# Kernel tuning notes

Hardware: AMD Instinct MI355X
Metric: run time of the kernel (lower is better)

The kernel has to match this reference:

```python
import jax, jax.numpy as jnp
import numpy as np

N = 100000   # nodes
E = 3200000  # edges (avg degree 32)
F = 128      # node_features
H = 128      # GCN hidden
A = 1024     # num_actions
B = 256      # graphs in batch


def setup_inputs() -> dict:
    key = jax.random.key(0)
    ks = jax.random.split(key, 11)
    glorot = lambda k, shp: (jax.random.normal(k, shp, jnp.float32)
                             / np.sqrt(float(shp[0])))
    return {
        "x": jax.random.normal(ks[0], (N, F), jnp.float32),
        "edge_index": jax.random.randint(ks[1], (2, E), 0, N, dtype=jnp.int64),
        "batch": jnp.sort(jax.random.randint(ks[2], (N,), 0, B, dtype=jnp.int64)),
        "W1": glorot(ks[3], (F, H)), "b1": jnp.zeros((H,), jnp.float32),
        "W2": glorot(ks[4], (H, H)), "b2": jnp.zeros((H,), jnp.float32),
        "Wv": glorot(ks[5], (H, 1)), "bv": jnp.zeros((1,), jnp.float32),
        "Wp": glorot(ks[6], (H, A)), "bp": jnp.zeros((A,), jnp.float32),
    }


def reference(x, edge_index, batch, W1, b1, W2, b2, Wv, bv, Wp, bp):
    # --- GCN normalization (PyG gcn_norm with self-loops) ---
    loops = jnp.arange(N, dtype=edge_index.dtype)
    src = jnp.concatenate([edge_index[0], loops])  # [E+N] message sources
    dst = jnp.concatenate([edge_index[1], loops])  # [E+N] aggregation targets
    deg = jax.ops.segment_sum(jnp.ones(src.shape, jnp.float32), dst,
                              num_segments=N)       # in-degree incl. self-loop
    dinv = jax.lax.rsqrt(deg)                       # deg >= 1 due to self-loops
    norm = (dinv[src] * dinv[dst])[:, None]         # [E+N, 1]

    def gcn_conv(h, W, b):
        h = h @ W                                   # transform first (small GEMM)
        agg = jax.ops.segment_sum(h[src] * norm, dst, num_segments=N)
        return agg + b

    h = jax.nn.relu(gcn_conv(x, W1, b1))
    h = jax.nn.relu(gcn_conv(h, W2, b2))

    # --- global_mean_pool over graph ids ---
    counts = jax.ops.segment_sum(jnp.ones((N,), jnp.float32), batch,
                                 num_segments=B)
    pooled = jax.ops.segment_sum(h, batch, num_segments=B) \
             / jnp.maximum(counts, 1.0)[:, None]    # [B, H]

    v = jnp.tanh(pooled @ Wv + bv)                  # [B, 1]
    p = jax.nn.softmax(pooled @ Wp + bp, axis=-1)   # [B, A]
    return (v, p)
```

## Files before the change

### kernel.cpp

```cpp
#include <hip/hip_runtime.h>
#include <hip/hip_bf16.h>

#define GN 100000
#define GE 3200000
#define GH 128
#define GA 1024
#define GB 256

#define NBUK 391
#define BCAP 12288
#define B1BLK 5120
#define NBIN1 625

typedef __attribute__((ext_vector_type(8))) short short8v;
typedef __attribute__((ext_vector_type(4))) float f32x4v;

__device__ __forceinline__ unsigned int f2bf(float f) {
    unsigned int u = __float_as_uint(f);
    return (u + 0x7fffu + ((u >> 16) & 1u)) >> 16;
}
__device__ __forceinline__ float bflo(unsigned int u) { return __uint_as_float(u << 16); }
__device__ __forceinline__ float bfhi(unsigned int u) { return __uint_as_float(u & 0xffff0000u); }

__device__ __forceinline__ int wswz(int k, int n) {
    return (((k >> 5) * 8 + (n >> 4)) * 64 + ((k >> 3) & 3) * 16 + (n & 15)) * 8 + (k & 7);
}

__global__ __launch_bounds__(256) void k_prep(const float* __restrict__ W1,
                                              const float* __restrict__ W2,
                                              unsigned short* __restrict__ Wsw1,
                                              unsigned short* __restrict__ Wsw2,
                                              int* __restrict__ gcur) {
    int b = blockIdx.x, t = threadIdx.x;
    if (b < 64) {
        int idx = b * 256 + t;
        int k = idx >> 7, n = idx & 127;
        Wsw1[wswz(k, n)] = (unsigned short)f2bf(W1[idx]);
    } else if (b < 128) {
        int idx = (b - 64) * 256 + t;
        int k = idx >> 7, n = idx & 127;
        Wsw2[wswz(k, n)] = (unsigned short)f2bf(W2[idx]);
    } else {
        for (int i = t; i < NBUK; i += 256) gcur[i] = i * BCAP;
    }
}

__global__ __launch_bounds__(256) void k_bin1(const int* __restrict__ src,
                                              const int* __restrict__ dst,
                                              int* __restrict__ gcur,
                                              unsigned int* __restrict__ binned) {
    __shared__ int hist[512], lstart[512];
    __shared__ int curl[NBUK], gbase[NBUK];
    __shared__ unsigned int srec[B1BLK];
    __shared__ unsigned short sbuk[B1BLK];
    __shared__ int wsc[4];
    int t = threadIdx.x;
    hist[t] = 0; hist[t + 256] = 0;
    __syncthreads();
    int beg = blockIdx.x * B1BLK;
    unsigned int rec[20]; int bukv[20];
#pragma unroll
    for (int k = 0; k < 20; k++) {
        int e = beg + t + k * 256;
        int d = dst[e];
        rec[k] = (unsigned int)src[e] | ((unsigned int)(d & 255) << 17);
        bukv[k] = d >> 8;
        atomicAdd(&hist[bukv[k]], 1);
    }
    __syncthreads();
    int v0 = hist[2 * t], v1 = hist[2 * t + 1];
    int s = v0 + v1;
    int lane = t & 63, w = t >> 6;
    int x = s;
#pragma unroll
    for (int off = 1; off < 64; off <<= 1) {
        int y = __shfl_up(x, off);
        if (lane >= off) x += y;
    }
    if (lane == 63) wsc[w] = x;
    __syncthreads();
    int wo = 0;
#pragma unroll
    for (int i = 0; i < 4; i++)
        if (i < w) wo += wsc[i];
    int excl = wo + x - s;
    lstart[2 * t] = excl;
    lstart[2 * t + 1] = excl + v0;
    __syncthreads();
    for (int i = t; i < NBUK; i += 256) {
        curl[i] = lstart[i];
        int c = hist[i];
        gbase[i] = c ? atomicAdd(&gcur[i], c) : 0;
    }
    __syncthreads();
#pragma unroll
    for (int k = 0; k < 20; k++) {
        int p = atomicAdd(&curl[bukv[k]], 1);
        srec[p] = rec[k];
        sbuk[p] = (unsigned short)bukv[k];
    }
    __syncthreads();
    for (int i = t; i < B1BLK; i += 256) {
        int b = sbuk[i];
        binned[gbase[b] + (i - lstart[b])] = srec[i];
    }
}

__global__ __launch_bounds__(256) void k_sort2(const unsigned int* __restrict__ binned,
                                               const int* __restrict__ gcur,
                                               int* __restrict__ csr_src,
                                               int* __restrict__ nbeg,
                                               int* __restrict__ nend,
                                               float* __restrict__ dinv) {
    int b = blockIdx.x, t = threadIdx.x;
    __shared__ int hist[256], cur[256], wsum[4];
    hist[t] = 0;
    __syncthreads();
    int rbase = b * BCAP;
    int rend = gcur[b];
    for (int e = rbase + t; e < rend; e += 256)
        atomicAdd(&hist[(binned[e] >> 17) & 255], 1);
    __syncthreads();
    int h = hist[t];
    int lane = t & 63, w = t >> 6;
    int x = h;
#pragma unroll
    for (int off = 1; off < 64; off <<= 1) {
        int y = __shfl_up(x, off);
        if (lane >= off) x += y;
    }
    if (lane == 63) wsum[w] = x;
    __syncthreads();
    int wo = 0;
#pragma unroll
    for (int i = 0; i < 4; i++)
        if (i < w) wo += wsum[i];
    int excl = wo + x - h;
    int node = (b << 8) + t;
    if (node < GN) {
        nbeg[node] = rbase + excl;
        nend[node] = rbase + excl + h;
        dinv[node] = rsqrtf((float)(h + 1));
    }
    cur[t] = excl;
    __syncthreads();
    for (int e = rbase + t; e < rend; e += 256) {
        unsigned int v = binned[e];
        int dl = (v >> 17) & 255;
        int p = atomicAdd(&cur[dl], 1);
        csr_src[rbase + p] = (int)(v & 0x1FFFF);
    }
}

__global__ __launch_bounds__(256) void k_gemm1(const float* __restrict__ A,
                                               const unsigned short* __restrict__ Wsw,
                                               const float* __restrict__ dinv,
                                               unsigned int* __restrict__ C) {
    __shared__ float Ct[64][128];
    int t = threadIdx.x;
    int row0 = blockIdx.x * 64;
    int wv = t >> 6, lane = t & 63;
    int m16 = lane & 15, g = lane >> 4;
    f32x4v acc[8];
#pragma unroll
    for (int nb = 0; nb < 8; nb++) acc[nb] = (f32x4v){0.f, 0.f, 0.f, 0.f};
    int arow = row0 + wv * 16 + m16; if (arow >= GN) arow = GN - 1;
#pragma unroll
    for (int kb = 0; kb < 4; kb++) {
        const float* ap = &A[(size_t)arow * 128 + kb * 32 + g * 8];
        float4 a0 = *(const float4*)ap;
        float4 a1 = *(const float4*)(ap + 4);
        uint4 up;
        up.x = f2bf(a0.x) | (f2bf(a0.y) << 16);
        up.y = f2bf(a0.z) | (f2bf(a0.w) << 16);
        up.z = f2bf(a1.x) | (f2bf(a1.y) << 16);
        up.w = f2bf(a1.z) | (f2bf(a1.w) << 16);
        short8v af = *(short8v*)&up;
#pragma unroll
        for (int nb = 0; nb < 8; nb++) {
            short8v bf = *(const short8v*)&Wsw[((kb * 8 + nb) * 64 + lane) * 8];
            acc[nb] = __builtin_amdgcn_mfma_f32_16x16x32_bf16(af, bf, acc[nb], 0, 0, 0);
        }
    }
#pragma unroll
    for (int nb = 0; nb < 8; nb++)
#pragma unroll
        for (int r = 0; r < 4; r++)
            Ct[wv * 16 + g * 4 + r][nb * 16 + m16] = acc[nb][r];
    __syncthreads();
    int lr = t >> 2, ch = t & 3;
    int grow = row0 + lr;
    if (grow < GN) {
        float dv = dinv[grow];
#pragma unroll
        for (int q = 0; q < 4; q++) {
            int c0 = ch * 32 + q * 8;
            uint4 po;
            po.x = f2bf(Ct[lr][c0 + 0] * dv) | (f2bf(Ct[lr][c0 + 1] * dv) << 16);
            po.y = f2bf(Ct[lr][c0 + 2] * dv) | (f2bf(Ct[lr][c0 + 3] * dv) << 16);
            po.z = f2bf(Ct[lr][c0 + 4] * dv) | (f2bf(Ct[lr][c0 + 5] * dv) << 16);
            po.w = f2bf(Ct[lr][c0 + 6] * dv) | (f2bf(Ct[lr][c0 + 7] * dv) << 16);
            *(uint4*)&C[(size_t)grow * 64 + ch * 16 + q * 4] = po;
        }
    }
}

__global__ __launch_bounds__(256) void k_gemm2(const unsigned int* __restrict__ A,
                                               const unsigned short* __restrict__ Wsw,
                                               const float* __restrict__ dinv,
                                               unsigned int* __restrict__ C) {
    __shared__ float Ct[64][128];
    int t = threadIdx.x;
    int row0 = blockIdx.x * 64;
    int wv = t >> 6, lane = t & 63;
    int m16 = lane & 15, g = lane >> 4;
    f32x4v acc[8];
#pragma unroll
    for (int nb = 0; nb < 8; nb++) acc[nb] = (f32x4v){0.f, 0.f, 0.f, 0.f};
    int arow = row0 + wv * 16 + m16; if (arow >= GN) arow = GN - 1;
#pragma unroll
    for (int kb = 0; kb < 4; kb++) {
        uint4 av = *(const uint4*)&A[(size_t)arow * 64 + kb * 16 + g * 4];
        short8v af = *(short8v*)&av;
#pragma unroll
        for (int nb = 0; nb < 8; nb++) {
            short8v bf = *(const short8v*)&Wsw[((kb * 8 + nb) * 64 + lane) * 8];
            acc[nb] = __builtin_amdgcn_mfma_f32_16x16x32_bf16(af, bf, acc[nb], 0, 0, 0);
        }
    }
#pragma unroll
    for (int nb = 0; nb < 8; nb++)
#pragma unroll
        for (int r = 0; r < 4; r++)
            Ct[wv * 16 + g * 4 + r][nb * 16 + m16] = acc[nb][r];
    __syncthreads();
    int lr = t >> 2, ch = t & 3;
    int grow = row0 + lr;
    if (grow < GN) {
        float dv = dinv[grow];
#pragma unroll
        for (int q = 0; q < 4; q++) {
            int c0 = ch * 32 + q * 8;
            uint4 po;
            po.x = f2bf(Ct[lr][c0 + 0] * dv) | (f2bf(Ct[lr][c0 + 1] * dv) << 16);
            po.y = f2bf(Ct[lr][c0 + 2] * dv) | (f2bf(Ct[lr][c0 + 3] * dv) << 16);
            po.z = f2bf(Ct[lr][c0 + 4] * dv) | (f2bf(Ct[lr][c0 + 5] * dv) << 16);
            po.w = f2bf(Ct[lr][c0 + 6] * dv) | (f2bf(Ct[lr][c0 + 7] * dv) << 16);
            *(uint4*)&C[(size_t)grow * 64 + ch * 16 + q * 4] = po;
        }
    }
}

__global__ __launch_bounds__(256) void k_aggregate(const unsigned int* __restrict__ ts,
                                                   const int* __restrict__ nbeg,
                                                   const int* __restrict__ nend,
                                                   const int* __restrict__ csr_src,
                                                   const float* __restrict__ dinv,
                                                   const float* __restrict__ bias,
                                                   unsigned int* __restrict__ out) {
    int node = blockIdx.x * 4 + (threadIdx.x >> 6);
    if (node >= GN) return;
    int lane = threadIdx.x & 63;
    int beg = nbeg[node];
    int end = nend[node];
    float di = dinv[node];
    float ax = 0.f, ay = 0.f;
    for (int base = beg; base < end; base += 64) {
        int n = end - base; if (n > 64) n = 64;
        int myidx = (lane < n) ? csr_src[base + lane] : 0;
        int k = 0;
        for (; k + 16 <= n; k += 16) {
            unsigned int u[16];
#pragma unroll
            for (int q = 0; q < 16; q++) {
                int s = __shfl(myidx, k + q);
                u[q] = ts[s * 64 + lane];
            }
#pragma unroll
            for (int q = 0; q < 16; q++) { ax += bflo(u[q]); ay += bfhi(u[q]); }
        }
        for (; k + 4 <= n; k += 4) {
            unsigned int u[4];
#pragma unroll
            for (int q = 0; q < 4; q++) {
                int s = __shfl(myidx, k + q);
                u[q] = ts[s * 64 + lane];
            }
#pragma unroll
            for (int q = 0; q < 4; q++) { ax += bflo(u[q]); ay += bfhi(u[q]); }
        }
        for (; k < n; k++) {
            int s = __shfl(myidx, k);
            unsigned int u = ts[s * 64 + lane];
            ax += bflo(u); ay += bfhi(u);
        }
    }
    unsigned int su = ts[(size_t)node * 64 + lane];
    float bx = bias[lane * 2 + 0], by = bias[lane * 2 + 1];
    float ox = fmaxf(fmaf(di, ax + bflo(su), bx), 0.f);
    float oy = fmaxf(fmaf(di, ay + bfhi(su), by), 0.f);
    out[(size_t)node * 64 + lane] = f2bf(ox) | (f2bf(oy) << 16);
}

__global__ __launch_bounds__(256) void k_pool(const unsigned int* __restrict__ h,
                                              const int* __restrict__ batch,
                                              float* __restrict__ pooled) {
    int g = blockIdx.x;
    int t = threadIdx.x;
    int f = t & 63, part = t >> 6;
    int lo = 0, hi = GN;
    while (lo < hi) { int m = (lo + hi) >> 1; if (batch[m] < g) lo = m + 1; else hi = m; }
    int start = lo;
    hi = GN;
    while (lo < hi) { int m = (lo + hi) >> 1; if (batch[m] <= g) lo = m + 1; else hi = m; }
    int end = lo;
    float ax = 0.f, ay = 0.f;
    for (int i = start + part; i < end; i += 4) {
        unsigned int u = h[(size_t)i * 64 + f];
        ax += bflo(u); ay += bfhi(u);
    }
    __shared__ float redx[256], redy[256];
    redx[t] = ax; redy[t] = ay;
    __syncthreads();
    if (part == 0) {
        float sx = redx[f] + redx[f + 64] + redx[f + 128] + redx[f + 192];
        float sy = redy[f] + redy[f + 64] + redy[f + 128] + redy[f + 192];
        float inv = 1.0f / fmaxf((float)(end - start), 1.0f);
        pooled[g * 128 + 2 * f + 0] = sx * inv;
        pooled[g * 128 + 2 * f + 1] = sy * inv;
    }
}

__global__ void k_value(const float* __restrict__ pooled, const float* __restrict__ Wv,
                        const float* __restrict__ bv, float* __restrict__ out) {
    int g = threadIdx.x;
    const float4* p4 = (const float4*)(pooled + g * 128);
    const float4* w4 = (const float4*)Wv;
    float s = 0.f;
#pragma unroll 8
    for (int i = 0; i < 32; i++) {
        float4 a = p4[i], b = w4[i];
        s += a.x * b.x + a.y * b.y + a.z * b.z + a.w * b.w;
    }
    out[g] = tanhf(s + bv[0]);
}

__global__ __launch_bounds__(256) void k_policy(const float* __restrict__ pooled,
                                                const float* __restrict__ Wp,
                                                const float* __restrict__ bp,
                                                float* __restrict__ out) {
    int g0 = blockIdx.x * 4;
    int t = threadIdx.x;
    __shared__ float pr[4][128];
    __shared__ float red[256];
    if (t < 128) {
#pragma unroll
        for (int gg = 0; gg < 4; gg++)
            pr[gg][t] = pooled[(size_t)(g0 + gg) * 128 + t];
    }
    __syncthreads();
    float bb0 = bp[t], bb1 = bp[t + 256], bb2 = bp[t + 512], bb3 = bp[t + 768];
    float acc[4][4];
#pragma unroll
    for (int gg = 0; gg < 4; gg++) {
        acc[gg][0] = bb0; acc[gg][1] = bb1; acc[gg][2] = bb2; acc[gg][3] = bb3;
    }
    for (int k = 0; k < 128; k++) {
        const float* wr = Wp + (size_t)k * 1024;
        float w0 = wr[t], w1 = wr[t + 256], w2 = wr[t + 512], w3 = wr[t + 768];
#pragma unroll
        for (int gg = 0; gg < 4; gg++) {
            float pv = pr[gg][k];
            acc[gg][0] = fmaf(pv, w0, acc[gg][0]);
            acc[gg][1] = fmaf(pv, w1, acc[gg][1]);
            acc[gg][2] = fmaf(pv, w2, acc[gg][2]);
            acc[gg][3] = fmaf(pv, w3, acc[gg][3]);
        }
    }
#pragma unroll
    for (int gg = 0; gg < 4; gg++) {
        float m = fmaxf(fmaxf(acc[gg][0], acc[gg][1]), fmaxf(acc[gg][2], acc[gg][3]));
        red[t] = m;
        __syncthreads();
        for (int off = 128; off > 0; off >>= 1) {
            if (t < off) red[t] = fmaxf(red[t], red[t + off]);
            __syncthreads();
        }
        float mx = red[0];
        __syncthreads();
        float e0 = __expf(acc[gg][0] - mx), e1 = __expf(acc[gg][1] - mx);
        float e2 = __expf(acc[gg][2] - mx), e3 = __expf(acc[gg][3] - mx);
        red[t] = (e0 + e1) + (e2 + e3);
        __syncthreads();
        for (int off = 128; off > 0; off >>= 1) {
            if (t < off) red[t] += red[t + off];
            __syncthreads();
        }
        float inv = 1.0f / red[0];
        __syncthreads();
        size_t ob = (size_t)(g0 + gg) * 1024;
        out[ob + t + 0]   = e0 * inv;
        out[ob + t + 256] = e1 * inv;
        out[ob + t + 512] = e2 * inv;
        out[ob + t + 768] = e3 * inv;
    }
}

extern "C" void kernel_launch(void* const* d_in, const int* in_sizes, int n_in,
                              void* d_out, int out_size, void* d_ws, size_t ws_size,
                              hipStream_t stream) {
    const float* x    = (const float*)d_in[0];
    const int*   ei   = (const int*)d_in[1];
    const int*   srcA = ei;
    const int*   dstA = ei + GE;
    const int*   batch = (const int*)d_in[2];
    const float* W1 = (const float*)d_in[3];
    const float* b1 = (const float*)d_in[4];
    const float* W2 = (const float*)d_in[5];
    const float* b2 = (const float*)d_in[6];
    const float* Wv = (const float*)d_in[7];
    const float* bv = (const float*)d_in[8];
    const float* Wp = (const float*)d_in[9];
    const float* bp = (const float*)d_in[10];
    float* out = (float*)d_out;

    char* ws = (char*)d_ws;
    unsigned int* bufH = (unsigned int*)ws;  ws += (size_t)GN * 64 * 4;
    unsigned int* ts_bf = (unsigned int*)ws; ws += (size_t)GN * 64 * 4;
    float* pooled = (float*)ws;      ws += (size_t)GB * 128 * 4;
    float* dinv = (float*)ws;        ws += (size_t)100352 * 4;
    int*   nbeg = (int*)ws;          ws += (size_t)100352 * 4;
    int*   nend = (int*)ws;          ws += (size_t)100352 * 4;
    int*   csr_src = (int*)ws;       ws += (size_t)NBUK * BCAP * 4;
    int*   gcur = (int*)ws;          ws += 512 * 4;
    unsigned short* Wsw1 = (unsigned short*)ws; ws += 16384 * 2;
    unsigned short* Wsw2 = (unsigned short*)ws; ws += 16384 * 2;
    unsigned int* binned = ts_bf;

    k_prep<<<129, 256, 0, stream>>>(W1, W2, Wsw1, Wsw2, gcur);
    k_bin1<<<NBIN1, 256, 0, stream>>>(srcA, dstA, gcur, binned);
    k_sort2<<<NBUK, 256, 0, stream>>>(binned, gcur, csr_src, nbeg, nend, dinv);

    k_gemm1<<<(GN + 63) / 64, 256, 0, stream>>>(x, Wsw1, dinv, ts_bf);
    k_aggregate<<<GN / 4, 256, 0, stream>>>(ts_bf, nbeg, nend, csr_src, dinv, b1, bufH);

    k_gemm2<<<(GN + 63) / 64, 256, 0, stream>>>(bufH, Wsw2, dinv, ts_bf);
    k_aggregate<<<GN / 4, 256, 0, stream>>>(ts_bf, nbeg, nend, csr_src, dinv, b2, bufH);

    k_pool<<<GB, 256, 0, stream>>>(bufH, batch, pooled);
    k_value<<<1, 256, 0, stream>>>(pooled, Wv, bv, out);
    k_policy<<<GB / 4, 256, 0, stream>>>(pooled, Wp, bp, out + GB);
}
```

Before: 372.8 us.

## Split aggregation into feature slices with 8 edges gathered per wave step

The aggregation kernel now splits the 64 packed-bf16 feature columns into 8 slices of 8 columns, one slice per block (blockIdx & 7). Each wave processes 8 edges at once, with each 8-lane group reading a 32-byte chunk of a source row. Groups are reduced at the end with xor shuffles. A persistent grid-stride loop runs over node quads. The aim is that concurrently running blocks touch only one column slice of the gathered table, improving cache locality, and that more edges are in flight per wave. In exchange, each row read becomes a small 32-byte access, the CSR indices are read 8 times (using nontemporal loads), and a cross-lane reduction is added.

```diff
diff --git a/kernel.cpp b/kernel.cpp
--- a/kernel.cpp
+++ b/kernel.cpp
@@ -258,48 +258,56 @@
                                                    const float* __restrict__ dinv,
                                                    const float* __restrict__ bias,
                                                    unsigned int* __restrict__ out) {
-    int node = blockIdx.x * 4 + (threadIdx.x >> 6);
-    if (node >= GN) return;
-    int lane = threadIdx.x & 63;
-    int beg = nbeg[node];
-    int end = nend[node];
-    float di = dinv[node];
-    float ax = 0.f, ay = 0.f;
-    for (int base = beg; base < end; base += 64) {
-        int n = end - base; if (n > 64) n = 64;
-        int myidx = (lane < n) ? csr_src[base + lane] : 0;
-        int k = 0;
-        for (; k + 16 <= n; k += 16) {
-            unsigned int u[16];
-#pragma unroll
-            for (int q = 0; q < 16; q++) {
-                int s = __shfl(myidx, k + q);
-                u[q] = ts[s * 64 + lane];
+    int slice = blockIdx.x & 7;
+    int qbase = blockIdx.x >> 3;
+    int wave = threadIdx.x >> 6, lane = threadIdx.x & 63;
+    int eg = lane >> 3, u = lane & 7;
+    int colu = slice * 8 + u;
+    float2 bb = *(const float2*)&bias[colu * 2];
+    for (int quad = qbase; quad < GN / 4; quad += 2048) {
+        int node = quad * 4 + wave;
+        int beg = nbeg[node], end = nend[node];
+        float di = dinv[node];
+        float ax = 0.f, ay = 0.f;
+        for (int base = beg; base < end; base += 64) {
+            int n = end - base; if (n > 64) n = 64;
+            int myidx = (lane < n) ? __builtin_nontemporal_load(&csr_src[base + lane]) : 0;
+            int k = 0;
+            for (; k + 32 <= n; k += 32) {
+                int s0 = __shfl(myidx, k + eg);
+                int s1 = __shfl(myidx, k + 8 + eg);
+                int s2 = __shfl(myidx, k + 16 + eg);
+                int s3 = __shfl(myidx, k + 24 + eg);
+                unsigned int v0 = ts[(size_t)s0 * 64 + colu];
+                unsigned int v1 = ts[(size_t)s1 * 64 + colu];
+                unsigned int v2 = ts[(size_t)s2 * 64 + colu];
+                unsigned int v3 = ts[(size_t)s3 * 64 + colu];
+                ax += (bflo(v0) + bflo(v1)) + (bflo(v2) + bflo(v3));
+                ay += (bfhi(v0) + bfhi(v1)) + (bfhi(v2) + bfhi(v3));
             }
-#pragma unroll
-            for (int q = 0; q < 16; q++) { ax += bflo(u[q]); ay += bfhi(u[q]); }
-        }
-        for (; k + 4 <= n; k += 4) {
-            unsigned int u[4];
-#pragma unroll
-            for (int q = 0; q < 4; q++) {
-                int s = __shfl(myidx, k + q);
-                u[q] = ts[s * 64 + lane];
+            for (; k + 8 <= n; k += 8) {
+                int s = __shfl(myidx, k + eg);
+                unsigned int v = ts[(size_t)s * 64 + colu];
+                ax += bflo(v); ay += bfhi(v);
             }
-#pragma unroll
-            for (int q = 0; q < 4; q++) { ax += bflo(u[q]); ay += bfhi(u[q]); }
-        }
-        for (; k < n; k++) {
-            int s = __shfl(myidx, k);
-            unsigned int u = ts[s * 64 + lane];
-            ax += bflo(u); ay += bfhi(u);
-        }
-    }
-    unsigned int su = ts[(size_t)node * 64 + lane];
-    float bx = bias[lane * 2 + 0], by = bias[lane * 2 + 1];
-    float ox = fmaxf(fmaf(di, ax + bflo(su), bx), 0.f);
-    float oy = fmaxf(fmaf(di, ay + bfhi(su), by), 0.f);
-    out[(size_t)node * 64 + lane] = f2bf(ox) | (f2bf(oy) << 16);
+            if (k < n) {
+                int j = k + eg;
+                int jj = (j < n) ? j : k;
+                int s = __shfl(myidx, jj);
+                unsigned int v = ts[(size_t)s * 64 + colu];
+                if (j < n) { ax += bflo(v); ay += bfhi(v); }
+            }
+        }
+        ax += __shfl_xor(ax, 8);  ay += __shfl_xor(ay, 8);
+        ax += __shfl_xor(ax, 16); ay += __shfl_xor(ay, 16);
+        ax += __shfl_xor(ax, 32); ay += __shfl_xor(ay, 32);
+        unsigned int sv = ts[(size_t)node * 64 + colu];
+        float ox = fmaxf(fmaf(di, ax + bflo(sv), bb.x), 0.f);
+        float oy = fmaxf(fmaf(di, ay + bfhi(sv), bb.y), 0.f);
+        if (eg == 0)
+            __builtin_nontemporal_store(f2bf(ox) | (f2bf(oy) << 16),
+                                        &out[(size_t)node * 64 + colu]);
+    }
 }
 
 __global__ __launch_bounds__(256) void k_pool(const unsigned int* __restrict__ h,
@@ -442,10 +450,10 @@
     k_sort2<<<NBUK, 256, 0, stream>>>(binned, gcur, csr_src, nbeg, nend, dinv);
 
     k_gemm1<<<(GN + 63) / 64, 256, 0, stream>>>(x, Wsw1, dinv, ts_bf);
-    k_aggregate<<<GN / 4, 256, 0, stream>>>(ts_bf, nbeg, nend, csr_src, dinv, b1, bufH);
+    k_aggregate<<<16384, 256, 0, stream>>>(ts_bf, nbeg, nend, csr_src, dinv, b1, bufH);
 
     k_gemm2<<<(GN + 63) / 64, 256, 0, stream>>>(bufH, Wsw2, dinv, ts_bf);
-    k_aggregate<<<GN / 4, 256, 0, stream>>>(ts_bf, nbeg, nend, csr_src, dinv, b2, bufH);
+    k_aggregate<<<16384, 256, 0, stream>>>(ts_bf, nbeg, nend, csr_src, dinv, b2, bufH);
 
     k_pool<<<GB, 256, 0, stream>>>(bufH, batch, pooled);
     k_value<<<1, 256, 0, stream>>>(pooled, Wv, bv, out);
```

Result: slower. 908.0 us (+143.6%).
